# Kernel optimization log

Measured on AMD Instinct MI355X. Metric: run time of the kernel, lower is better.

## Reference

```python
import jax, jax.numpy as jnp
import numpy as np

B, T, E, D, A, O, L = 16, 512, 1024, 1024, 1024, 10000, 128
SOS = EOS = O - 1
SCALING = 2.0  # AttDot softmax scaling in espnet of this era


def setup_inputs() -> dict:
    key = jax.random.key(0)
    ks = jax.random.split(key, 16)
    s = 0.05
    inp = {
        "hpad": jax.random.normal(ks[0], (B, T, E), jnp.float32),
        "hlen": jnp.full((B,), T, dtype=jnp.int32),
        "ys": jax.random.randint(ks[1], (B, L), 0, O - 2).astype(jnp.int32),
        "embed_w": jax.random.normal(ks[2], (O, D), jnp.float32) * s,
        "att_Wenc": jax.random.normal(ks[3], (E, A), jnp.float32) * s,
        "att_Wdec": jax.random.normal(ks[4], (D, A), jnp.float32) * s,
        "W_ih0": jax.random.normal(ks[5], (4 * D, D + E), jnp.float32) * s,
        "W_hh0": jax.random.normal(ks[6], (4 * D, D), jnp.float32) * s,
        "b_ih0": jnp.zeros((4 * D,), jnp.float32),
        "b_hh0": jnp.zeros((4 * D,), jnp.float32),
        "W_ih1": jax.random.normal(ks[7], (4 * D, D), jnp.float32) * s,
        "W_hh1": jax.random.normal(ks[8], (4 * D, D), jnp.float32) * s,
        "b_ih1": jnp.zeros((4 * D,), jnp.float32),
        "b_hh1": jnp.zeros((4 * D,), jnp.float32),
        "W_out": jax.random.normal(ks[9], (D, O), jnp.float32) * s,
        "b_out": jnp.zeros((O,), jnp.float32),
    }
    return inp


def _lstm_cell(x, h, c, W_ih, W_hh, b_ih, b_hh):
    g = x @ W_ih.T + b_ih + h @ W_hh.T + b_hh
    i, f, gg, o = jnp.split(g, 4, axis=-1)
    c_new = jax.nn.sigmoid(f) * c + jax.nn.sigmoid(i) * jnp.tanh(gg)
    h_new = jax.nn.sigmoid(o) * jnp.tanh(c_new)
    return h_new, c_new


def reference(hpad, hlen, ys, embed_w, att_Wenc, att_Wdec,
              W_ih0, W_hh0, b_ih0, b_hh0, W_ih1, W_hh1, b_ih1, b_hh1,
              W_out, b_out):
    b, t, e = hpad.shape
    d = W_hh0.shape[1]
    # mask_by_length(hpad, hlen, 0)
    mask = (jnp.arange(t)[None, :] < hlen[:, None])
    hpad_m = hpad * mask[..., None].astype(hpad.dtype)

    # sos/eos padding: pad_ys_in = [sos; y], pad_ys_out = [y; eos]
    sos_col = jnp.full((b, 1), SOS, dtype=ys.dtype)
    eos_col = jnp.full((b, 1), EOS, dtype=ys.dtype)
    ys_in = jnp.concatenate([sos_col, ys], axis=1)   # [B, L+1]
    ys_out = jnp.concatenate([ys, eos_col], axis=1)  # [B, L+1]
    olength = ys_in.shape[1]

    eys = embed_w[ys_in]                 # [B, L+1, D]
    pre_enc = jnp.tanh(jnp.einsum('bte,ea->bta', hpad_m, att_Wenc))  # [B,T,A]

    def step(carry, ey):
        z0, c0, z1, c1 = carry
        # AttDot: e = sum(tanh(Wenc h) * tanh(Wdec z0)); w = softmax(2*e)
        dq = jnp.tanh(z0 @ att_Wdec)                        # [B, A]
        escore = jnp.einsum('bta,ba->bt', pre_enc, dq)      # [B, T]
        w = jax.nn.softmax(SCALING * escore, axis=1)
        att_c = jnp.einsum('bt,bte->be', w, hpad_m)         # [B, E]
        x0 = jnp.concatenate([ey, att_c], axis=1)           # [B, D+E]
        z0, c0 = _lstm_cell(x0, z0, c0, W_ih0, W_hh0, b_ih0, b_hh0)
        z1, c1 = _lstm_cell(z0, z1, c1, W_ih1, W_hh1, b_ih1, b_hh1)
        return (z0, c0, z1, c1), z1

    zeros = jnp.zeros((b, d), hpad.dtype)
    carry0 = (zeros, zeros, zeros, zeros)
    _, z_all = jax.lax.scan(step, carry0, jnp.swapaxes(eys, 0, 1))  # [L+1, B, D]
    z_all = jnp.swapaxes(z_all, 0, 1).reshape(b * olength, d)

    logits = z_all @ W_out + b_out                          # [B*(L+1), O]
    labels = ys_out.reshape(-1)
    logp = jax.nn.log_softmax(logits, axis=-1)
    nll = -jnp.take_along_axis(logp, labels[:, None], axis=1)[:, 0]
    # all sequences have length L, no ignore_id padding; loss *= mean(len(ys_in)) - 1 = L
    loss = jnp.mean(nll) * jnp.float32(olength - 1)
    acc = jnp.mean((jnp.argmax(logits, axis=-1) == labels).astype(jnp.float32))
    return loss, acc
```

## Files before the change

### kernel.cpp

```cpp
#include <hip/hip_runtime.h>
#include <math.h>

#define NB 16
#define NT 512
#define NE 1024
#define ND 1024
#define NA 1024
#define NO 10000
#define NL 128
#define NOL 129
#define NROWS (NB*NOL)
#define TOK_SOS 9999
#define TOK_EOS 9999
#define NBLK 256

typedef unsigned short u16;
typedef unsigned int u32;
typedef __bf16 bf16x8 __attribute__((ext_vector_type(8)));
typedef float f32x4 __attribute__((ext_vector_type(4)));
typedef unsigned short u16x8 __attribute__((ext_vector_type(8)));
typedef unsigned short u16x4 __attribute__((ext_vector_type(4)));

__device__ __forceinline__ float sigf(float x){ return 1.0f/(1.0f+expf(-x)); }
__device__ __forceinline__ float b2f(u16 s){
  union { u32 i; float f; } u; u.i = ((u32)s) << 16; return u.f;
}
__device__ __forceinline__ u16 f2b(float f){
  union { float f; u32 i; } u; u.f = f;
  u32 r = u.i + 0x7FFFu + ((u.i >> 16) & 1u);
  return (u16)(r >> 16);
}
__device__ __forceinline__ bf16x8 cvt8(float4 a, float4 b){
  union { u16 u[8]; bf16x8 v; } c;
  c.u[0]=f2b(a.x); c.u[1]=f2b(a.y); c.u[2]=f2b(a.z); c.u[3]=f2b(a.w);
  c.u[4]=f2b(b.x); c.u[5]=f2b(b.y); c.u[6]=f2b(b.z); c.u[7]=f2b(b.w);
  return c.v;
}
__device__ __forceinline__ bf16x8 zero8(){
  union { u16 u[8]; bf16x8 v; } c;
  #pragma unroll
  for (int i=0;i<8;++i) c.u[i]=0;
  return c.v;
}

__device__ __forceinline__ void coh_stf(float* p, float v){
  __hip_atomic_store(p, v, __ATOMIC_RELAXED, __HIP_MEMORY_SCOPE_AGENT);
}
__device__ __forceinline__ u32 coh_ldu(const u32* p){
  return __hip_atomic_load((u32*)p, __ATOMIC_RELAXED, __HIP_MEMORY_SCOPE_AGENT);
}
__device__ __forceinline__ void coh_stu(u32* p, u32 v){
  __hip_atomic_store(p, v, __ATOMIC_RELAXED, __HIP_MEMORY_SCOPE_AGENT);
}
__device__ __forceinline__ float dot8(bf16x8 a, bf16x8 b){
  float s = 0.f;
  #pragma unroll
  for (int j=0;j<8;++j) s += (float)a[j]*(float)b[j];
  return s;
}

__global__ void zero4_kernel(uint4* __restrict__ p, int n){
  int i = blockIdx.x*256 + threadIdx.x;
  if (i < n) p[i] = make_uint4(0,0,0,0);
}

__global__ __launch_bounds__(256) void cvt_nk_kernel(
    const float* __restrict__ src, int ld, int off, u16* __restrict__ dst){
  int i = (blockIdx.x*256 + threadIdx.x)*4;
  int row = i >> 10, col = i & 1023;
  float4 v = *(const float4*)(src + (size_t)row*ld + off + col);
  u16x4 o = { f2b(v.x), f2b(v.y), f2b(v.z), f2b(v.w) };
  *(u16x4*)(dst + i) = o;
}

__global__ __launch_bounds__(256) void tcvt_kernel(
    const float* __restrict__ src, int R, int C, u16* __restrict__ dst){
  __shared__ float tile[32][33];
  const int c0 = blockIdx.x*32, r0 = blockIdx.y*32;
  const int tx = threadIdx.x & 31, ty = threadIdx.x >> 5;
  #pragma unroll
  for (int k = 0; k < 4; ++k){
    int rr = ty + k*8;
    int c = c0 + tx;
    float v = (c < C) ? src[(size_t)(r0+rr)*C + c] : 0.0f;
    tile[rr][tx] = v;
  }
  __syncthreads();
  #pragma unroll
  for (int k = 0; k < 4; ++k){
    int cc = ty + k*8;
    dst[(size_t)(c0+cc)*R + r0 + tx] = f2b(tile[tx][cc]);
  }
}

__global__ __launch_bounds__(256) void hpadT_kernel(
    const float* __restrict__ hpad, const int* __restrict__ hlen, u16* __restrict__ dst){
  __shared__ float tile[32][33];
  const int e0 = blockIdx.x*32, t0 = blockIdx.y*32, b = blockIdx.z;
  const int tx = threadIdx.x & 31, ty = threadIdx.x >> 5;
  const int len = hlen[b];
  #pragma unroll
  for (int k = 0; k < 4; ++k){
    int r = ty + k*8;
    tile[r][tx] = hpad[((size_t)b*512 + t0 + r)*1024 + e0 + tx];
  }
  __syncthreads();
  #pragma unroll
  for (int k = 0; k < 4; ++k){
    int el = ty + k*8;
    float m = (t0 + tx < len) ? 1.0f : 0.0f;
    dst[((size_t)b*1024 + e0 + el)*512 + t0 + tx] = f2b(tile[tx][el]*m);
  }
}

__global__ void bias_add_kernel(const float* __restrict__ a, const float* __restrict__ b,
                                float* __restrict__ o){
  int i = blockIdx.x*256 + threadIdx.x;
  if (i < 4096) o[i] = a[i] + b[i];
}

__global__ __launch_bounds__(256) void preenc_mfma(
    const float* __restrict__ hpad, const int* __restrict__ hlen,
    const u16* __restrict__ wencT, u16* __restrict__ pre){
  const int m0 = blockIdx.x*64, n0 = blockIdx.y*64;
  const int tid = threadIdx.x, lane = tid & 63, wv = tid >> 6;
  const int r = lane & 15, q = lane >> 4;
  const int ar = m0 + wv*16 + r;
  const bool on = (ar & 511) < hlen[ar >> 9];
  const float* ap = hpad + (size_t)ar*1024 + q*8;
  f32x4 acc[4] = {{0,0,0,0},{0,0,0,0},{0,0,0,0},{0,0,0,0}};
  for (int kt = 0; kt < 32; ++kt){
    bf16x8 a;
    if (on){
      float4 v0 = *(const float4*)(ap + kt*32);
      float4 v1 = *(const float4*)(ap + kt*32 + 4);
      a = cvt8(v0, v1);
    } else a = zero8();
    #pragma unroll
    for (int s = 0; s < 4; ++s){
      const u16* bp = wencT + (size_t)(n0 + s*16 + r)*1024 + kt*32 + q*8;
      acc[s] = __builtin_amdgcn_mfma_f32_16x16x32_bf16(a, *(const bf16x8*)bp, acc[s], 0,0,0);
    }
  }
  #pragma unroll
  for (int s = 0; s < 4; ++s)
    #pragma unroll
    for (int rr = 0; rr < 4; ++rr){
      int row = m0 + wv*16 + q*4 + rr, col = n0 + s*16 + r;
      pre[(size_t)row*1024 + col] = f2b(tanhf(acc[s][rr]));
    }
}

__global__ __launch_bounds__(256) void gey_mfma(
    const int* __restrict__ ys, const float* __restrict__ embed,
    const float* __restrict__ Wih0, const float* __restrict__ bih0,
    const float* __restrict__ bhh0, u16* __restrict__ gey){
  const int m0 = blockIdx.x*64, n0 = blockIdx.y*64;
  const int tid = threadIdx.x, lane = tid & 63, wv = tid >> 6;
  const int r = lane & 15, q = lane >> 4;
  const int ar = m0 + wv*16 + r;
  int tok = 0;
  if (ar < NROWS){
    int bb = ar / NOL, l = ar - bb*NOL;
    tok = (l==0) ? TOK_SOS : ys[bb*NL + l - 1];
  }
  const float* ap = embed + (size_t)tok*1024 + q*8;
  f32x4 acc[4] = {{0,0,0,0},{0,0,0,0},{0,0,0,0},{0,0,0,0}};
  for (int kt = 0; kt < 32; ++kt){
    float4 v0 = *(const float4*)(ap + kt*32);
    float4 v1 = *(const float4*)(ap + kt*32 + 4);
    bf16x8 a = cvt8(v0, v1);
    #pragma unroll
    for (int s = 0; s < 4; ++s){
      const float* bp = Wih0 + (size_t)(n0 + s*16 + r)*2048 + kt*32 + q*8;
      float4 w0 = *(const float4*)(bp);
      float4 w1 = *(const float4*)(bp + 4);
      acc[s] = __builtin_amdgcn_mfma_f32_16x16x32_bf16(a, cvt8(w0,w1), acc[s], 0,0,0);
    }
  }
  #pragma unroll
  for (int s = 0; s < 4; ++s)
    #pragma unroll
    for (int rr = 0; rr < 4; ++rr){
      int row = m0 + wv*16 + q*4 + rr, col = n0 + s*16 + r;
      if (row < NROWS)
        gey[(size_t)row*4096 + col] = f2b(acc[s][rr] + bih0[col] + bhh0[col]);
    }
}

__global__ __launch_bounds__(256) void logits_mfma(
    const u16* __restrict__ zallb, const u16* __restrict__ woutT,
    const float* __restrict__ bout, u16* __restrict__ logits){
  const int m0 = blockIdx.x*64, n0 = blockIdx.y*64;
  const int tid = threadIdx.x, lane = tid & 63, wv = tid >> 6;
  const int r = lane & 15, q = lane >> 4;
  const int ar = m0 + wv*16 + r;
  const u16* ap = zallb + (size_t)ar*1024 + q*8;
  f32x4 acc[4] = {{0,0,0,0},{0,0,0,0},{0,0,0,0},{0,0,0,0}};
  for (int kt = 0; kt < 32; ++kt){
    bf16x8 a = *(const bf16x8*)(ap + kt*32);
    #pragma unroll
    for (int s = 0; s < 4; ++s){
      const u16* bp = woutT + (size_t)(n0 + s*16 + r)*1024 + kt*32 + q*8;
      acc[s] = __builtin_amdgcn_mfma_f32_16x16x32_bf16(a, *(const bf16x8*)bp, acc[s], 0,0,0);
    }
  }
  #pragma unroll
  for (int s = 0; s < 4; ++s)
    #pragma unroll
    for (int rr = 0; rr < 4; ++rr){
      int row = m0 + wv*16 + q*4 + rr, col = n0 + s*16 + r;
      if (row < NROWS && col < NO)
        logits[(size_t)row*NO + col] = f2b(acc[s][rr] + bout[col]);
    }
}

__device__ __forceinline__ void gbar(u32* af, int epoch){
  __syncthreads();
  if (blockIdx.x == 0){
    int w = threadIdx.x;
    if (w > 0){
      while (coh_ldu(&af[w << 5]) < (u32)epoch) __builtin_amdgcn_s_sleep(1);
    }
    __syncthreads();
    if (threadIdx.x == 0) coh_stu(&af[0], (u32)epoch);
  } else {
    if (threadIdx.x == 0){
      coh_stu(&af[blockIdx.x << 5], (u32)epoch);
      while (coh_ldu(&af[0]) < (u32)epoch) __builtin_amdgcn_s_sleep(1);
    }
    __syncthreads();
  }
}

__device__ __forceinline__ f32x4 tile_gemm(const u16* lw, const u16* ab){
  f32x4 acc = {0.f,0.f,0.f,0.f};
  #pragma unroll
  for (int kt = 0; kt < 16; ++kt){
    bf16x8 a = *(const bf16x8*)(ab + kt*32);
    bf16x8 b = *(const bf16x8*)(lw + kt*512);
    acc = __builtin_amdgcn_mfma_f32_16x16x32_bf16(a, b, acc, 0, 0, 0);
  }
  return acc;
}

__global__ __launch_bounds__(256, 1) void seq_kernel(
    const u16* __restrict__ pre,
    const u16* __restrict__ hpadT,
    const u16* __restrict__ w0c, const u16* __restrict__ wh0,
    const u16* __restrict__ w1c, const u16* __restrict__ wh1,
    const u16* __restrict__ wdecT,
    const u16* __restrict__ gey,
    const float* __restrict__ bias1,
    const int* __restrict__ hlen,
    u16* dqr,
    float* escr,
    u16* attcr,
    u16* z0r,
    u16* z1r,
    u16* zallb,
    u32* af)
{
  __builtin_amdgcn_fence(__ATOMIC_ACQUIRE, "agent");

  const int wg = blockIdx.x, tid = threadIdx.x;
  const int lane = tid & 63, wv = tid >> 6;
  const int r = lane & 15, q = lane >> 4;

  extern __shared__ __align__(16) u16 dynlds[];
  u16* lw1 = dynlds;
  u16* lw0 = dynlds + 32768;
  __shared__ float sred[256];
  __shared__ float sw[512];
  __shared__ float spart[4][64];
  __shared__ float gex[4][16][16];
  __shared__ float sdq[16*16*4];

  const int dg16 = (wg & 63)*16, sub4 = (wg >> 6)*4;

  #pragma unroll
  for (int it = 0; it < 16; ++it){
    int m = tid + it*256;
    int kb = m >> 4, c = m & 15;
    int k0 = kb*8;
    int gi = c >> 2;
    int d  = dg16 + sub4 + (c & 3);
    size_t gr = (size_t)(gi*1024 + d)*1024;
    const u16* s1 = (k0 < 1024) ? (w1c + gr + k0) : (wh1 + gr + k0 - 1024);
    const u16* s0 = (k0 < 1024) ? (w0c + gr + k0) : (wh0 + gr + k0 - 1024);
    *(u16x8*)(lw1 + (m << 3)) = *(const u16x8*)s1;
    *(u16x8*)(lw0 + (m << 3)) = *(const u16x8*)s0;
  }
  __syncthreads();

  float c0r = 0.f, c1r = 0.f;
  int epoch = 1;
  const int lwoff = ((wv*64 + q)*16 + r) << 3;

  for (int t = 0; t <= NOL; ++t){
    const u16* z0t = z0r + (size_t)t*16384;
    u16* dq_t   = dqr   + (size_t)t*16384;
    float* esc_t= escr  + (size_t)t*8192;
    u16* attc_t = attcr + (size_t)t*16384;

    if (t >= 1){
      const int s = t - 1;
      const u16* z1p = z1r + (size_t)(t-1)*16384;
      const u16* ab = ((wv < 2) ? z0t : z1p) + r*1024 + (wv & 1)*512 + q*8;
      f32x4 acc = tile_gemm(lw1 + lwoff, ab);
      #pragma unroll
      for (int rr = 0; rr < 4; ++rr) gex[wv][q*4+rr][r] = acc[rr];
      __syncthreads();
      if (tid < 64){
        int b = tid >> 2, dd = tid & 3, d = dg16 + sub4 + dd;
        float g0 = gex[0][b][0*4+dd] + gex[1][b][0*4+dd] + gex[2][b][0*4+dd] + gex[3][b][0*4+dd];
        float g1 = gex[0][b][1*4+dd] + gex[1][b][1*4+dd] + gex[2][b][1*4+dd] + gex[3][b][1*4+dd];
        float g2 = gex[0][b][2*4+dd] + gex[1][b][2*4+dd] + gex[2][b][2*4+dd] + gex[3][b][2*4+dd];
        float g3 = gex[0][b][3*4+dd] + gex[1][b][3*4+dd] + gex[2][b][3*4+dd] + gex[3][b][3*4+dd];
        g0 += bias1[d]; g1 += bias1[1024+d]; g2 += bias1[2048+d]; g3 += bias1[3072+d];
        float cn = sigf(g1)*c1r + sigf(g0)*tanhf(g2);
        float zn = sigf(g3)*tanhf(cn);
        c1r = cn;
        float zn2 = __shfl_down(zn, 1);
        if ((tid & 1) == 0){
          u32 pk = (u32)f2b(zn) | ((u32)f2b(zn2) << 16);
          *(u32*)(zallb + ((size_t)b*NOL + s)*1024 + d) = pk;
          coh_stu((u32*)(z1r + (size_t)t*16384 + b*1024 + d), pk);
        }
      }
      __syncthreads();
    }
    if (t < NOL){
      const int b = tid & 15, ks = tid >> 4;
      float a4[4] = {0.f,0.f,0.f,0.f};
      #pragma unroll
      for (int i = 0; i < 8; ++i){
        bf16x8 za = *(const bf16x8*)(z0t + b*1024 + ks*64 + i*8);
        #pragma unroll
        for (int nn = 0; nn < 4; ++nn){
          bf16x8 wb = *(const bf16x8*)(wdecT + (size_t)(wg*4+nn)*1024 + ks*64 + i*8);
          a4[nn] += dot8(za, wb);
        }
      }
      #pragma unroll
      for (int nn = 0; nn < 4; ++nn) sdq[(ks*16 + b)*4 + nn] = a4[nn];
      __syncthreads();
      if (tid < 64){
        int b2 = tid >> 2, nn = tid & 3;
        float s2 = 0.f;
        #pragma unroll
        for (int ks2 = 0; ks2 < 16; ++ks2) s2 += sdq[(ks2*16 + b2)*4 + nn];
        float dv = tanhf(s2);
        float dv2 = __shfl_down(dv, 1);
        if ((tid & 1) == 0){
          u32 pk = (u32)f2b(dv) | ((u32)f2b(dv2) << 16);
          coh_stu((u32*)(dq_t + b2*1024 + wg*4 + nn), pk);
        }
      }
    }
    gbar(af, epoch++);
    if (t == NOL) break;

    {
      const int rbase = wg*32 + wv*8;
      const int b = (wg*32) >> 9;
      const u16* dqb = dq_t + b*1024 + lane*16;
      u16x8 d0 = *(const u16x8*)(dqb);
      u16x8 d1 = *(const u16x8*)(dqb + 8);
      float qv[16];
      #pragma unroll
      for (int j = 0; j < 8; ++j){ qv[j] = b2f(d0[j]); qv[8+j] = b2f(d1[j]); }
      #pragma unroll
      for (int rr = 0; rr < 8; ++rr){
        const u16* pr = pre + (size_t)(rbase+rr)*1024 + lane*16;
        u16x8 p0 = *(const u16x8*)(pr);
        u16x8 p1 = *(const u16x8*)(pr+8);
        float acc = 0.f;
        #pragma unroll
        for (int j = 0; j < 8; ++j){
          acc += b2f(p0[j])*qv[j];
          acc += b2f(p1[j])*qv[8+j];
        }
        #pragma unroll
        for (int off = 32; off > 0; off >>= 1) acc += __shfl_xor(acc, off, 64);
        if (lane == 0) coh_stf(&esc_t[rbase+rr], 2.0f*acc);
      }
    }
    gbar(af, epoch++);

    {
      const int b = wg >> 4, ec = wg & 15;
      const int len = hlen[b];
      float e0 = (tid < len)     ? esc_t[b*512 + tid]       : -INFINITY;
      float e1 = (tid+256 < len) ? esc_t[b*512 + tid + 256] : -INFINITY;
      sred[tid] = fmaxf(e0, e1);
      __syncthreads();
      #pragma unroll
      for (int s2 = 128; s2 > 0; s2 >>= 1){
        if (tid < s2) sred[tid] = fmaxf(sred[tid], sred[tid+s2]);
        __syncthreads();
      }
      float mx = sred[0];
      __syncthreads();
      float p0 = (tid < len)     ? expf(e0 - mx) : 0.0f;
      float p1 = (tid+256 < len) ? expf(e1 - mx) : 0.0f;
      sred[tid] = p0 + p1;
      __syncthreads();
      #pragma unroll
      for (int s2 = 128; s2 > 0; s2 >>= 1){
        if (tid < s2) sred[tid] += sred[tid+s2];
        __syncthreads();
      }
      float inv = 1.0f/sred[0];
      sw[tid] = p0*inv; sw[tid+256] = p1*inv;
      __syncthreads();
      const int el = tid & 63, th = tid >> 6;
      const u16* hp = hpadT + ((size_t)b*1024 + ec*64 + el)*512 + th*128;
      float acc = 0.f;
      #pragma unroll
      for (int i = 0; i < 16; ++i){
        u16x8 v = *(const u16x8*)(hp + i*8);
        #pragma unroll
        for (int j = 0; j < 8; ++j) acc += sw[th*128 + i*8 + j]*b2f(v[j]);
      }
      spart[th][el] = acc;
      __syncthreads();
      if (tid < 64){
        float s2 = spart[0][tid]+spart[1][tid]+spart[2][tid]+spart[3][tid];
        float s2n = __shfl_down(s2, 1);
        if ((tid & 1) == 0){
          u32 pk = (u32)f2b(s2) | ((u32)f2b(s2n) << 16);
          coh_stu((u32*)(attc_t + b*1024 + ec*64 + tid), pk);
        }
      }
    }
    gbar(af, epoch++);

    {
      const u16* ab = ((wv < 2) ? attc_t : z0t) + r*1024 + (wv & 1)*512 + q*8;
      f32x4 acc = tile_gemm(lw0 + lwoff, ab);
      #pragma unroll
      for (int rr = 0; rr < 4; ++rr) gex[wv][q*4+rr][r] = acc[rr];
      __syncthreads();
      if (tid < 64){
        int b = tid >> 2, dd = tid & 3, d = dg16 + sub4 + dd;
        const u16* gr = gey + ((size_t)b*NOL + t)*4096 + d;
        float g0 = gex[0][b][0*4+dd] + gex[1][b][0*4+dd] + gex[2][b][0*4+dd] + gex[3][b][0*4+dd];
        float g1 = gex[0][b][1*4+dd] + gex[1][b][1*4+dd] + gex[2][b][1*4+dd] + gex[3][b][1*4+dd];
        float g2 = gex[0][b][2*4+dd] + gex[1][b][2*4+dd] + gex[2][b][2*4+dd] + gex[3][b][2*4+dd];
        float g3 = gex[0][b][3*4+dd] + gex[1][b][3*4+dd] + gex[2][b][3*4+dd] + gex[3][b][3*4+dd];
        g0 += b2f(gr[0]); g1 += b2f(gr[1024]); g2 += b2f(gr[2048]); g3 += b2f(gr[3072]);
        float cn = sigf(g1)*c0r + sigf(g0)*tanhf(g2);
        float zn = sigf(g3)*tanhf(cn);
        c0r = cn;
        float zn2 = __shfl_down(zn, 1);
        if ((tid & 1) == 0){
          u32 pk = (u32)f2b(zn) | ((u32)f2b(zn2) << 16);
          coh_stu((u32*)(z0r + (size_t)(t+1)*16384 + b*1024 + d), pk);
        }
      }
    }
    gbar(af, epoch++);
  }
}

__global__ __launch_bounds__(256) void loss_kernel(
    const u16* __restrict__ logits, const int* __restrict__ ys, float* __restrict__ accum){
  int row = blockIdx.x;
  int tid = threadIdx.x;
  const u16* lr = logits + (size_t)row * NO;
  __shared__ float sv[256];
  __shared__ int   si[256];
  float mx = -INFINITY; int mi = 0;
  for (int n = tid; n < NO; n += 256){
    float v = b2f(lr[n]);
    if (v > mx){ mx = v; mi = n; }
  }
  sv[tid] = mx; si[tid] = mi;
  __syncthreads();
  for (int s=128; s>0; s>>=1){
    if (tid < s){
      if (sv[tid+s] > sv[tid] || (sv[tid+s]==sv[tid] && si[tid+s] < si[tid])){
        sv[tid] = sv[tid+s]; si[tid] = si[tid+s];
      }
    }
    __syncthreads();
  }
  float gmx = sv[0]; int gmi = si[0];
  __syncthreads();
  float ps = 0.0f;
  for (int n = tid; n < NO; n += 256) ps += expf(b2f(lr[n])-gmx);
  sv[tid] = ps;
  __syncthreads();
  for (int s=128; s>0; s>>=1){ if (tid<s) sv[tid] += sv[tid+s]; __syncthreads(); }
  if (tid==0){
    int b = row / NOL, l = row - b*NOL;
    int label = (l < NL) ? ys[b*NL + l] : TOK_EOS;
    float lse = gmx + logf(sv[0]);
    float nll = lse - b2f(lr[label]);
    atomicAdd(&accum[0], nll);
    atomicAdd(&accum[1], (gmi==label) ? 1.0f : 0.0f);
  }
}

__global__ void finalize_kernel(const float* __restrict__ accum, float* __restrict__ out){
  out[0] = accum[0] / (float)NROWS * (float)(NOL-1);
  out[1] = accum[1] / (float)NROWS;
}

extern "C" void kernel_launch(void* const* d_in, const int* in_sizes, int n_in,
                              void* d_out, int out_size, void* d_ws, size_t ws_size,
                              hipStream_t stream){
  const float* hpad  = (const float*)d_in[0];
  const int*   hlen  = (const int*)  d_in[1];
  const int*   ys    = (const int*)  d_in[2];
  const float* embed = (const float*)d_in[3];
  const float* Wenc  = (const float*)d_in[4];
  const float* Wdec  = (const float*)d_in[5];
  const float* Wih0  = (const float*)d_in[6];
  const float* Whh0  = (const float*)d_in[7];
  const float* bih0  = (const float*)d_in[8];
  const float* bhh0  = (const float*)d_in[9];
  const float* Wih1  = (const float*)d_in[10];
  const float* Whh1  = (const float*)d_in[11];
  const float* bih1  = (const float*)d_in[12];
  const float* bhh1  = (const float*)d_in[13];
  const float* Wout  = (const float*)d_in[14];
  const float* bout  = (const float*)d_in[15];
  float* out = (float*)d_out;

  char* ws = (char*)d_ws;
  size_t cur = 0;
  auto alloc = [&](size_t bytes) -> char* {
    char* p = ws + cur;
    cur += (bytes + 255) & ~(size_t)255;
    return p;
  };
  u16*   pre_bf   = (u16*)  alloc(16777216);
  u16*   hpadT    = (u16*)  alloc(16777216);
  u16*   w0c      = (u16*)  alloc(8388608);
  u16*   wh0      = (u16*)  alloc(8388608);
  u16*   w1c      = (u16*)  alloc(8388608);
  u16*   wh1      = (u16*)  alloc(8388608);
  u16*   wdecT    = (u16*)  alloc(2097152);
  u16*   wencT    = (u16*)  alloc(2097152);
  u16*   woutT    = (u16*)  alloc(20578304);
  u16*   gey      = (u16*)  alloc(16908288);
  u16*   zallb    = (u16*)  alloc(4325376);
  u16*   logits   = (u16*)  alloc(41280000);
  float* bias1    = (float*)alloc(16384);
  u16*   dqr      = (u16*)  alloc(129u*32768);
  float* escr     = (float*)alloc(129u*32768);
  u16*   attcr    = (u16*)  alloc(129u*32768);
  u16*   z0r      = (u16*)  alloc(130u*32768);
  u16*   z1r      = (u16*)  alloc(130u*32768);
  u32*   af       = (u32*)  alloc(32768);
  float* accum    = (float*)alloc(128);

  zero4_kernel<<<9, 256, 0, stream>>>((uint4*)af, 2056);
  zero4_kernel<<<8, 256, 0, stream>>>((uint4*)z0r, 2048);
  zero4_kernel<<<8, 256, 0, stream>>>((uint4*)z1r, 2048);

  tcvt_kernel<<<dim3(32,32),  256, 0, stream>>>(Wenc, 1024, 1024, wencT);
  tcvt_kernel<<<dim3(32,32),  256, 0, stream>>>(Wdec, 1024, 1024, wdecT);
  tcvt_kernel<<<dim3(313,32), 256, 0, stream>>>(Wout, 1024, NO,   woutT);
  cvt_nk_kernel<<<4096, 256, 0, stream>>>(Wih0, 2048, 1024, w0c);
  cvt_nk_kernel<<<4096, 256, 0, stream>>>(Whh0, 1024, 0, wh0);
  cvt_nk_kernel<<<4096, 256, 0, stream>>>(Wih1, 1024, 0, w1c);
  cvt_nk_kernel<<<4096, 256, 0, stream>>>(Whh1, 1024, 0, wh1);
  hpadT_kernel<<<dim3(32,16,16), 256, 0, stream>>>(hpad, hlen, hpadT);
  bias_add_kernel<<<16, 256, 0, stream>>>(bih1, bhh1, bias1);
  preenc_mfma<<<dim3(128,16), 256, 0, stream>>>(hpad, hlen, wencT, pre_bf);
  gey_mfma<<<dim3(33,64), 256, 0, stream>>>(ys, embed, Wih0, bih0, bhh0, gey);

  hipFuncSetAttribute((const void*)seq_kernel,
                      hipFuncAttributeMaxDynamicSharedMemorySize, 131072);
  seq_kernel<<<NBLK, 256, 131072, stream>>>(pre_bf, hpadT, w0c, wh0, w1c, wh1,
                                            wdecT, gey, bias1, hlen,
                                            dqr, escr, attcr, z0r, z1r, zallb, af);

  logits_mfma<<<dim3(33,157), 256, 0, stream>>>(zallb, woutT, bout, logits);
  loss_kernel<<<NROWS, 256, 0, stream>>>(logits, ys, accum);
  finalize_kernel<<<1, 1, 0, stream>>>(accum, out);
}
```

Measured before the change: 4.106 ms.

## Retile GEMMs to 128x128 with bf16 prepasses, group barrier, online-softmax loss

```diff
diff --git a/kernel.cpp b/kernel.cpp
--- a/kernel.cpp
+++ b/kernel.cpp
@@ -30,17 +30,11 @@
   u32 r = u.i + 0x7FFFu + ((u.i >> 16) & 1u);
   return (u16)(r >> 16);
 }
-__device__ __forceinline__ bf16x8 cvt8(float4 a, float4 b){
-  union { u16 u[8]; bf16x8 v; } c;
-  c.u[0]=f2b(a.x); c.u[1]=f2b(a.y); c.u[2]=f2b(a.z); c.u[3]=f2b(a.w);
-  c.u[4]=f2b(b.x); c.u[5]=f2b(b.y); c.u[6]=f2b(b.z); c.u[7]=f2b(b.w);
-  return c.v;
-}
-__device__ __forceinline__ bf16x8 zero8(){
-  union { u16 u[8]; bf16x8 v; } c;
-  #pragma unroll
-  for (int i=0;i<8;++i) c.u[i]=0;
-  return c.v;
+__device__ __forceinline__ float dot8(bf16x8 a, bf16x8 b){
+  float s = 0.f;
+  #pragma unroll
+  for (int j=0;j<8;++j) s += (float)a[j]*(float)b[j];
+  return s;
 }
 
 __device__ __forceinline__ void coh_stf(float* p, float v){
@@ -51,12 +45,6 @@
 }
 __device__ __forceinline__ void coh_stu(u32* p, u32 v){
   __hip_atomic_store(p, v, __ATOMIC_RELAXED, __HIP_MEMORY_SCOPE_AGENT);
-}
-__device__ __forceinline__ float dot8(bf16x8 a, bf16x8 b){
-  float s = 0.f;
-  #pragma unroll
-  for (int j=0;j<8;++j) s += (float)a[j]*(float)b[j];
-  return s;
 }
 
 __global__ void zero4_kernel(uint4* __restrict__ p, int n){
@@ -93,6 +81,17 @@
   }
 }
 
+__global__ __launch_bounds__(256) void hpadbf_kernel(
+    const float* __restrict__ hpad, const int* __restrict__ hlen, u16* __restrict__ dst){
+  int i = (blockIdx.x*256 + threadIdx.x)*4;
+  int bt = i >> 10;
+  int b = bt >> 9, tt = bt & 511;
+  float4 v = *(const float4*)(hpad + (size_t)i);
+  float m = (tt < hlen[b]) ? 1.0f : 0.0f;
+  u16x4 o = { f2b(v.x*m), f2b(v.y*m), f2b(v.z*m), f2b(v.w*m) };
+  *(u16x4*)(dst + i) = o;
+}
+
 __global__ __launch_bounds__(256) void hpadT_kernel(
     const float* __restrict__ hpad, const int* __restrict__ hlen, u16* __restrict__ dst){
   __shared__ float tile[32][33];
@@ -119,100 +118,90 @@
   if (i < 4096) o[i] = a[i] + b[i];
 }
 
-__global__ __launch_bounds__(256) void preenc_mfma(
-    const float* __restrict__ hpad, const int* __restrict__ hlen,
-    const u16* __restrict__ wencT, u16* __restrict__ pre){
-  const int m0 = blockIdx.x*64, n0 = blockIdx.y*64;
-  const int tid = threadIdx.x, lane = tid & 63, wv = tid >> 6;
-  const int r = lane & 15, q = lane >> 4;
-  const int ar = m0 + wv*16 + r;
-  const bool on = (ar & 511) < hlen[ar >> 9];
-  const float* ap = hpad + (size_t)ar*1024 + q*8;
-  f32x4 acc[4] = {{0,0,0,0},{0,0,0,0},{0,0,0,0},{0,0,0,0}};
-  for (int kt = 0; kt < 32; ++kt){
-    bf16x8 a;
-    if (on){
-      float4 v0 = *(const float4*)(ap + kt*32);
-      float4 v1 = *(const float4*)(ap + kt*32 + 4);
-      a = cvt8(v0, v1);
-    } else a = zero8();
+__global__ __launch_bounds__(256) void eys_kernel(
+    const int* __restrict__ ys, const float* __restrict__ embed, u16* __restrict__ eys){
+  int row = blockIdx.x;
+  int c = threadIdx.x*4;
+  if (row < NROWS){
+    int b = row / NOL, l = row - b*NOL;
+    int tok = (l==0) ? TOK_SOS : ys[b*NL + l - 1];
+    float4 v = *(const float4*)(embed + (size_t)tok*1024 + c);
+    u16x4 o = { f2b(v.x), f2b(v.y), f2b(v.z), f2b(v.w) };
+    *(u16x4*)(eys + (size_t)row*1024 + c) = o;
+  } else {
+    u16x4 o = {0,0,0,0};
+    *(u16x4*)(eys + (size_t)row*1024 + c) = o;
+  }
+}
+
+#define GEMM128_BODY(Aptr, Bptr) \
+  const int tid = threadIdx.x, lane = tid & 63, wv = tid >> 6; \
+  const int r = lane & 15, q = lane >> 4; \
+  const int m0 = blockIdx.x*128, n0 = blockIdx.y*128; \
+  const int ar0 = m0 + wv*32 + r; \
+  f32x4 acc[2][8]; \
+  _Pragma("unroll") \
+  for (int a = 0; a < 2; ++a) \
+    _Pragma("unroll") \
+    for (int s = 0; s < 8; ++s) acc[a][s] = (f32x4){0.f,0.f,0.f,0.f}; \
+  const u16* a0p = (Aptr) + (size_t)ar0*1024 + q*8; \
+  const u16* a1p = a0p + 16*1024; \
+  const u16* bp  = (Bptr) + (size_t)(n0 + r)*1024 + q*8; \
+  for (int kt = 0; kt < 32; ++kt){ \
+    bf16x8 av0 = *(const bf16x8*)(a0p + kt*32); \
+    bf16x8 av1 = *(const bf16x8*)(a1p + kt*32); \
+    _Pragma("unroll") \
+    for (int s = 0; s < 8; ++s){ \
+      bf16x8 bv = *(const bf16x8*)(bp + (size_t)s*16384 + kt*32); \
+      acc[0][s] = __builtin_amdgcn_mfma_f32_16x16x32_bf16(av0, bv, acc[0][s], 0,0,0); \
+      acc[1][s] = __builtin_amdgcn_mfma_f32_16x16x32_bf16(av1, bv, acc[1][s], 0,0,0); \
+    } \
+  }
+
+__global__ __launch_bounds__(256) void preenc_g(
+    const u16* __restrict__ hpadbf, const u16* __restrict__ wencT, u16* __restrict__ pre){
+  GEMM128_BODY(hpadbf, wencT)
+  #pragma unroll
+  for (int a = 0; a < 2; ++a)
     #pragma unroll
-    for (int s = 0; s < 4; ++s){
-      const u16* bp = wencT + (size_t)(n0 + s*16 + r)*1024 + kt*32 + q*8;
-      acc[s] = __builtin_amdgcn_mfma_f32_16x16x32_bf16(a, *(const bf16x8*)bp, acc[s], 0,0,0);
-    }
-  }
-  #pragma unroll
-  for (int s = 0; s < 4; ++s)
+    for (int s = 0; s < 8; ++s)
+      #pragma unroll
+      for (int rr = 0; rr < 4; ++rr){
+        int row = m0 + wv*32 + a*16 + q*4 + rr, col = n0 + s*16 + r;
+        pre[(size_t)row*1024 + col] = f2b(tanhf(acc[a][s][rr]));
+      }
+}
+
+__global__ __launch_bounds__(256) void gey_g(
+    const u16* __restrict__ eys, const u16* __restrict__ w0e,
+    const float* __restrict__ bih0, const float* __restrict__ bhh0, u16* __restrict__ gey){
+  GEMM128_BODY(eys, w0e)
+  #pragma unroll
+  for (int a = 0; a < 2; ++a)
     #pragma unroll
-    for (int rr = 0; rr < 4; ++rr){
-      int row = m0 + wv*16 + q*4 + rr, col = n0 + s*16 + r;
-      pre[(size_t)row*1024 + col] = f2b(tanhf(acc[s][rr]));
-    }
-}
-
-__global__ __launch_bounds__(256) void gey_mfma(
-    const int* __restrict__ ys, const float* __restrict__ embed,
-    const float* __restrict__ Wih0, const float* __restrict__ bih0,
-    const float* __restrict__ bhh0, u16* __restrict__ gey){
-  const int m0 = blockIdx.x*64, n0 = blockIdx.y*64;
-  const int tid = threadIdx.x, lane = tid & 63, wv = tid >> 6;
-  const int r = lane & 15, q = lane >> 4;
-  const int ar = m0 + wv*16 + r;
-  int tok = 0;
-  if (ar < NROWS){
-    int bb = ar / NOL, l = ar - bb*NOL;
-    tok = (l==0) ? TOK_SOS : ys[bb*NL + l - 1];
-  }
-  const float* ap = embed + (size_t)tok*1024 + q*8;
-  f32x4 acc[4] = {{0,0,0,0},{0,0,0,0},{0,0,0,0},{0,0,0,0}};
-  for (int kt = 0; kt < 32; ++kt){
-    float4 v0 = *(const float4*)(ap + kt*32);
-    float4 v1 = *(const float4*)(ap + kt*32 + 4);
-    bf16x8 a = cvt8(v0, v1);
-    #pragma unroll
-    for (int s = 0; s < 4; ++s){
-      const float* bp = Wih0 + (size_t)(n0 + s*16 + r)*2048 + kt*32 + q*8;
-      float4 w0 = *(const float4*)(bp);
-      float4 w1 = *(const float4*)(bp + 4);
-      acc[s] = __builtin_amdgcn_mfma_f32_16x16x32_bf16(a, cvt8(w0,w1), acc[s], 0,0,0);
-    }
-  }
-  #pragma unroll
-  for (int s = 0; s < 4; ++s)
-    #pragma unroll
-    for (int rr = 0; rr < 4; ++rr){
-      int row = m0 + wv*16 + q*4 + rr, col = n0 + s*16 + r;
-      if (row < NROWS)
-        gey[(size_t)row*4096 + col] = f2b(acc[s][rr] + bih0[col] + bhh0[col]);
-    }
-}
-
-__global__ __launch_bounds__(256) void logits_mfma(
+    for (int s = 0; s < 8; ++s)
+      #pragma unroll
+      for (int rr = 0; rr < 4; ++rr){
+        int row = m0 + wv*32 + a*16 + q*4 + rr, col = n0 + s*16 + r;
+        if (row < NROWS)
+          gey[(size_t)row*4096 + col] = f2b(acc[a][s][rr] + bih0[col] + bhh0[col]);
+      }
+}
+
+__global__ __launch_bounds__(256) void logits_g(
     const u16* __restrict__ zallb, const u16* __restrict__ woutT,
     const float* __restrict__ bout, u16* __restrict__ logits){
-  const int m0 = blockIdx.x*64, n0 = blockIdx.y*64;
-  const int tid = threadIdx.x, lane = tid & 63, wv = tid >> 6;
-  const int r = lane & 15, q = lane >> 4;
-  const int ar = m0 + wv*16 + r;
-  const u16* ap = zallb + (size_t)ar*1024 + q*8;
-  f32x4 acc[4] = {{0,0,0,0},{0,0,0,0},{0,0,0,0},{0,0,0,0}};
-  for (int kt = 0; kt < 32; ++kt){
-    bf16x8 a = *(const bf16x8*)(ap + kt*32);
+  GEMM128_BODY(zallb, woutT)
+  #pragma unroll
+  for (int a = 0; a < 2; ++a)
     #pragma unroll
-    for (int s = 0; s < 4; ++s){
-      const u16* bp = woutT + (size_t)(n0 + s*16 + r)*1024 + kt*32 + q*8;
-      acc[s] = __builtin_amdgcn_mfma_f32_16x16x32_bf16(a, *(const bf16x8*)bp, acc[s], 0,0,0);
-    }
-  }
-  #pragma unroll
-  for (int s = 0; s < 4; ++s)
-    #pragma unroll
-    for (int rr = 0; rr < 4; ++rr){
-      int row = m0 + wv*16 + q*4 + rr, col = n0 + s*16 + r;
-      if (row < NROWS && col < NO)
-        logits[(size_t)row*NO + col] = f2b(acc[s][rr] + bout[col]);
-    }
+    for (int s = 0; s < 8; ++s)
+      #pragma unroll
+      for (int rr = 0; rr < 4; ++rr){
+        int row = m0 + wv*32 + a*16 + q*4 + rr, col = n0 + s*16 + r;
+        if (row < NROWS && col < NO)
+          logits[(size_t)row*NO + col] = f2b(acc[a][s][rr] + bout[col]);
+      }
 }
 
 __device__ __forceinline__ void gbar(u32* af, int epoch){
@@ -231,6 +220,16 @@
     }
     __syncthreads();
   }
+}
+
+__device__ __forceinline__ void group_bar(u32* gfl, int epoch){
+  __syncthreads();
+  if (threadIdx.x == 0) coh_stu(&gfl[blockIdx.x << 5], (u32)epoch);
+  const int base = blockIdx.x & ~15;
+  if ((int)threadIdx.x < 16){
+    while ((int)coh_ldu(&gfl[(base + threadIdx.x) << 5]) < epoch) __builtin_amdgcn_s_sleep(1);
+  }
+  __syncthreads();
 }
 
 __device__ __forceinline__ f32x4 tile_gemm(const u16* lw, const u16* ab){
@@ -259,7 +258,7 @@
     u16* z0r,
     u16* z1r,
     u16* zallb,
-    u32* af)
+    u32* af, u32* gfl)
 {
   __builtin_amdgcn_fence(__ATOMIC_ACQUIRE, "agent");
 
@@ -386,7 +385,7 @@
         if (lane == 0) coh_stf(&esc_t[rbase+rr], 2.0f*acc);
       }
     }
-    gbar(af, epoch++);
+    group_bar(gfl, epoch++);
 
     {
       const int b = wg >> 4, ec = wg & 15;
@@ -469,37 +468,38 @@
   int row = blockIdx.x;
   int tid = threadIdx.x;
   const u16* lr = logits + (size_t)row * NO;
-  __shared__ float sv[256];
+  __shared__ float sm[256], ss[256];
   __shared__ int   si[256];
-  float mx = -INFINITY; int mi = 0;
+  float m = -INFINITY, s = 0.f; int mi = 0x7FFFFFFF;
   for (int n = tid; n < NO; n += 256){
     float v = b2f(lr[n]);
-    if (v > mx){ mx = v; mi = n; }
-  }
-  sv[tid] = mx; si[tid] = mi;
-  __syncthreads();
-  for (int s=128; s>0; s>>=1){
-    if (tid < s){
-      if (sv[tid+s] > sv[tid] || (sv[tid+s]==sv[tid] && si[tid+s] < si[tid])){
-        sv[tid] = sv[tid+s]; si[tid] = si[tid+s];
-      }
+    if (v > m){
+      s = s*__expf(m - v) + 1.0f;
+      m = v; mi = n;
+    } else {
+      s += __expf(v - m);
+    }
+  }
+  sm[tid] = m; ss[tid] = s; si[tid] = mi;
+  __syncthreads();
+  for (int st = 128; st > 0; st >>= 1){
+    if (tid < st){
+      float m1 = sm[tid], s1 = ss[tid]; int i1 = si[tid];
+      float m2 = sm[tid+st], s2 = ss[tid+st]; int i2 = si[tid+st];
+      float M = fmaxf(m1, m2);
+      ss[tid] = s1*__expf(m1 - M) + s2*__expf(m2 - M);
+      sm[tid] = M;
+      si[tid] = (m1 > m2) ? i1 : (m2 > m1) ? i2 : min(i1, i2);
     }
     __syncthreads();
   }
-  float gmx = sv[0]; int gmi = si[0];
-  __syncthreads();
-  float ps = 0.0f;
-  for (int n = tid; n < NO; n += 256) ps += expf(b2f(lr[n])-gmx);
-  sv[tid] = ps;
-  __syncthreads();
-  for (int s=128; s>0; s>>=1){ if (tid<s) sv[tid] += sv[tid+s]; __syncthreads(); }
-  if (tid==0){
+  if (tid == 0){
     int b = row / NOL, l = row - b*NOL;
     int label = (l < NL) ? ys[b*NL + l] : TOK_EOS;
-    float lse = gmx + logf(sv[0]);
+    float lse = sm[0] + logf(ss[0]);
     float nll = lse - b2f(lr[label]);
     atomicAdd(&accum[0], nll);
-    atomicAdd(&accum[1], (gmi==label) ? 1.0f : 0.0f);
+    atomicAdd(&accum[1], (si[0]==label) ? 1.0f : 0.0f);
   }
 }
 
@@ -544,9 +544,9 @@
   u16*   wh1      = (u16*)  alloc(8388608);
   u16*   wdecT    = (u16*)  alloc(2097152);
   u16*   wencT    = (u16*)  alloc(2097152);
-  u16*   woutT    = (u16*)  alloc(20578304);
+  u16*   woutT    = (u16*)  alloc(20709376);
   u16*   gey      = (u16*)  alloc(16908288);
-  u16*   zallb    = (u16*)  alloc(4325376);
+  u16*   zallb    = (u16*)  alloc(4456448);
   u16*   logits   = (u16*)  alloc(41280000);
   float* bias1    = (float*)alloc(16384);
   u16*   dqr      = (u16*)  alloc(129u*32768);
@@ -555,31 +555,40 @@
   u16*   z0r      = (u16*)  alloc(130u*32768);
   u16*   z1r      = (u16*)  alloc(130u*32768);
   u32*   af       = (u32*)  alloc(32768);
+  u32*   gfl      = (u32*)  alloc(32768);
   float* accum    = (float*)alloc(128);
 
-  zero4_kernel<<<9, 256, 0, stream>>>((uint4*)af, 2056);
+  u16*   hpad_bf  = (u16*)logits;
+  u16*   eys      = (u16*)(logits + 8388608);
+  u16*   w0e      = (u16*)(logits + 11165696);
+
+  zero4_kernel<<<17, 256, 0, stream>>>((uint4*)af, 4104);
   zero4_kernel<<<8, 256, 0, stream>>>((uint4*)z0r, 2048);
   zero4_kernel<<<8, 256, 0, stream>>>((uint4*)z1r, 2048);
 
   tcvt_kernel<<<dim3(32,32),  256, 0, stream>>>(Wenc, 1024, 1024, wencT);
   tcvt_kernel<<<dim3(32,32),  256, 0, stream>>>(Wdec, 1024, 1024, wdecT);
-  tcvt_kernel<<<dim3(313,32), 256, 0, stream>>>(Wout, 1024, NO,   woutT);
+  tcvt_kernel<<<dim3(316,32), 256, 0, stream>>>(Wout, 1024, NO,   woutT);
   cvt_nk_kernel<<<4096, 256, 0, stream>>>(Wih0, 2048, 1024, w0c);
   cvt_nk_kernel<<<4096, 256, 0, stream>>>(Whh0, 1024, 0, wh0);
   cvt_nk_kernel<<<4096, 256, 0, stream>>>(Wih1, 1024, 0, w1c);
   cvt_nk_kernel<<<4096, 256, 0, stream>>>(Whh1, 1024, 0, wh1);
+  cvt_nk_kernel<<<4096, 256, 0, stream>>>(Wih0, 2048, 0, w0e);
+  hpadbf_kernel<<<8192, 256, 0, stream>>>(hpad, hlen, hpad_bf);
   hpadT_kernel<<<dim3(32,16,16), 256, 0, stream>>>(hpad, hlen, hpadT);
   bias_add_kernel<<<16, 256, 0, stream>>>(bih1, bhh1, bias1);
-  preenc_mfma<<<dim3(128,16), 256, 0, stream>>>(hpad, hlen, wencT, pre_bf);
-  gey_mfma<<<dim3(33,64), 256, 0, stream>>>(ys, embed, Wih0, bih0, bhh0, gey);
+  eys_kernel<<<2176, 256, 0, stream>>>(ys, embed, eys);
+
+  preenc_g<<<dim3(64, 8),  256, 0, stream>>>(hpad_bf, wencT, pre_bf);
+  gey_g   <<<dim3(17, 32), 256, 0, stream>>>(eys, w0e, bih0, bhh0, gey);
 
   hipFuncSetAttribute((const void*)seq_kernel,
                       hipFuncAttributeMaxDynamicSharedMemorySize, 131072);
   seq_kernel<<<NBLK, 256, 131072, stream>>>(pre_bf, hpadT, w0c, wh0, w1c, wh1,
                                             wdecT, gey, bias1, hlen,
-                                            dqr, escr, attcr, z0r, z1r, zallb, af);
-
-  logits_mfma<<<dim3(33,157), 256, 0, stream>>>(zallb, woutT, bout, logits);
+                                            dqr, escr, attcr, z0r, z1r, zallb, af, gfl);
+
+  logits_g<<<dim3(17, 79), 256, 0, stream>>>(zallb, woutT, bout, logits);
   loss_kernel<<<NROWS, 256, 0, stream>>>(logits, ys, accum);
   finalize_kernel<<<1, 1, 0, stream>>>(accum, out);
 }
```

Result: faster. 3.565 ms (-13.2%).
